# Performance work log

Hardware: AMD Instinct MI355X
Metric: run time of the kernel (lower is better)

The kernel has to match this reference:

```python
import jax, jax.numpy as jnp
import numpy as np

N = 65536      # nodes
E = 262144     # edges per metapath
K = 8          # sampled edges per node
NMP = 2        # metapaths (n_mp)
DEPTH = 2      # layers
H = 4          # heads
D = 256        # prep_len / hidden (= H*PH)
PH = 64        # per-head output dim
ED = 64        # raw edge embedding dim


def setup_inputs() -> dict:
    key = jax.random.key(0)
    ks = jax.random.split(key, 16)
    s = 1.0 / np.sqrt(D)
    return {
        "feats": jax.random.normal(ks[0], (N, D), jnp.float32),
        "edge_emb": jax.random.normal(ks[1], (NMP, E, ED), jnp.float32),
        "edge_node_adj": jax.random.randint(ks[2], (NMP, E, 2), 0, N, dtype=jnp.int32),
        "node2edge_idx": jax.random.randint(ks[3], (NMP, N, K), 0, E, dtype=jnp.int32),
        "W_prep0": jax.random.normal(ks[4], (D, D), jnp.float32) * s,
        "W_prep1": jax.random.normal(ks[5], (D, D), jnp.float32) * s,
        "W_eprep": jax.random.normal(ks[6], (NMP, ED, D), jnp.float32) * (1.0 / np.sqrt(ED)),
        "a_e": jax.random.normal(ks[7], (NMP, DEPTH, H, D), jnp.float32) * s,
        "a_n": jax.random.normal(ks[8], (NMP, DEPTH, H, D), jnp.float32) * s,
        "W_e": jax.random.normal(ks[9], (NMP, DEPTH, H, D, PH), jnp.float32) * s,
        "a_s": jax.random.normal(ks[10], (NMP, DEPTH, H, D), jnp.float32) * s,
        "a_edge": jax.random.normal(ks[11], (NMP, DEPTH, H, D), jnp.float32) * s,
        "W_self": jax.random.normal(ks[12], (NMP, DEPTH, H, D, PH), jnp.float32) * s,
        "W_nb": jax.random.normal(ks[13], (NMP, DEPTH, H, D, PH), jnp.float32) * s,
    }


def _forward(feats, edge_emb, edge_node_adj, node2edge_idx,
             W_prep0, W_prep1, W_eprep, a_e, a_n, W_e, a_s, a_edge, W_self, W_nb):
    dummy = feats @ W_prep0     # prep(layer_idx=0)  [N,D]
    base = feats @ W_prep1      # prep(layer_idx=1)  [N,D]
    outputs = []
    for mp in range(NMP):
        x = base
        edges = edge_emb[mp] @ W_eprep[mp]           # [E,D]
        ena = edge_node_adj[mp]                      # [E,2]
        n2e = node2edge_idx[mp]                      # [N,K]
        skips = []
        for L in range(DEPTH):
            # --- edge aggregator: gather 2 endpoint node feats, attend, project ---
            ep = x[ena]                              # [E,2,D] gather
            s_e = jax.nn.leaky_relu(
                jnp.einsum('eqd,hd->ehq', ep, a_n[mp, L])
                + jnp.einsum('ed,hd->eh', edges, a_e[mp, L])[..., None], 0.2)  # [E,H,2]
            alp = jax.nn.softmax(s_e, axis=-1)
            agg = jnp.einsum('ehq,eqd->ehd', alp, ep)                          # [E,H,D]
            e_out = jax.nn.elu(
                jnp.einsum('ehd,hdp->ehp', edges[:, None, :] + agg, W_e[mp, L])
            ).reshape(E, H * PH)                                               # [E,D]
            # --- node aggregator: gather K sampled edge feats (OLD edges), attend ---
            xin = x if L > 0 else dummy              # layer 0 self-feature uses dummy prep
            eg = edges[n2e]                          # [N,K,D] gather
            s_n = jax.nn.leaky_relu(
                jnp.einsum('nd,hd->nh', xin, a_s[mp, L])[:, :, None]
                + jnp.einsum('nkd,hd->nhk', eg, a_edge[mp, L]), 0.2)           # [N,H,K]
            aln = jax.nn.softmax(s_n, axis=-1)
            nag = jnp.einsum('nhk,nkd->nhd', aln, eg)                          # [N,H,D]
            n_out = jax.nn.elu(
                jnp.einsum('nd,hdp->nhp', xin, W_self[mp, L])
                + jnp.einsum('nhd,hdp->nhp', nag, W_nb[mp, L])
            ).reshape(N, H * PH)                                               # [N,D]
            skips.append(n_out)
            x = n_out
            edges = e_out
        outputs.append(jnp.concatenate(skips, axis=-1))   # [N, DEPTH*D]
    return jnp.stack(outputs, axis=0)                     # [NMP, N, DEPTH*D]


def reference(feats, edge_emb, edge_node_adj, node2edge_idx,
              W_prep0, W_prep1, W_eprep, a_e, a_n, W_e, a_s, a_edge, W_self, W_nb):
    return _forward(feats, edge_emb, edge_node_adj, node2edge_idx,
                    W_prep0, W_prep1, W_eprep, a_e, a_n, W_e, a_s, a_edge, W_self, W_nb)
```

## Files before the change

kernel.cpp:

```cpp
#include <hip/hip_runtime.h>

typedef unsigned short ushort_t;
typedef unsigned int uint_t;

#define N_NODES 65536
#define N_EDGES 262144

typedef __attribute__((ext_vector_type(8))) short bf16x8;
typedef __attribute__((ext_vector_type(4))) float f32x4;

__device__ __forceinline__ ushort_t f2b(float x) {
  uint_t u = __float_as_uint(x);
  u += 0x7fffu + ((u >> 16) & 1u);
  return (ushort_t)(u >> 16);
}
__device__ __forceinline__ void dec8(uint4 v, float* f) {
  f[0] = __uint_as_float(v.x << 16); f[1] = __uint_as_float(v.x & 0xffff0000u);
  f[2] = __uint_as_float(v.y << 16); f[3] = __uint_as_float(v.y & 0xffff0000u);
  f[4] = __uint_as_float(v.z << 16); f[5] = __uint_as_float(v.z & 0xffff0000u);
  f[6] = __uint_as_float(v.w << 16); f[7] = __uint_as_float(v.w & 0xffff0000u);
}
__device__ __forceinline__ void dec4(uint2 v, float* f) {
  f[0] = __uint_as_float(v.x << 16); f[1] = __uint_as_float(v.x & 0xffff0000u);
  f[2] = __uint_as_float(v.y << 16); f[3] = __uint_as_float(v.y & 0xffff0000u);
}
__device__ __forceinline__ uint4 enc8(const float* f) {
  uint4 v;
  v.x = (uint_t)f2b(f[0]) | ((uint_t)f2b(f[1]) << 16);
  v.y = (uint_t)f2b(f[2]) | ((uint_t)f2b(f[3]) << 16);
  v.z = (uint_t)f2b(f[4]) | ((uint_t)f2b(f[5]) << 16);
  v.w = (uint_t)f2b(f[6]) | ((uint_t)f2b(f[7]) << 16);
  return v;
}
__device__ __forceinline__ uint2 enc4(const float* f) {
  uint2 v;
  v.x = (uint_t)f2b(f[0]) | ((uint_t)f2b(f[1]) << 16);
  v.y = (uint_t)f2b(f[2]) | ((uint_t)f2b(f[3]) << 16);
  return v;
}
__device__ __forceinline__ void ld8(const float* p, float* f) {
  float4 v0 = *(const float4*)p;
  float4 v1 = *(const float4*)(p + 4);
  f[0]=v0.x; f[1]=v0.y; f[2]=v0.z; f[3]=v0.w;
  f[4]=v1.x; f[5]=v1.y; f[6]=v1.z; f[7]=v1.w;
}

#define ELUF(v) ((v) > 0.f ? (v) : __expf(v) - 1.f)

__device__ __forceinline__ void async16(void* lds, const void* g) {
  __builtin_amdgcn_global_load_lds(
      (const __attribute__((address_space(1))) void*)g,
      (__attribute__((address_space(3))) void*)lds, 16, 0, 0);
}

__global__ void wt_kernel(const float* __restrict__ src, ushort_t* __restrict__ dst,
                          int K, int N) {
  long m = blockIdx.y;
  long base = m * (long)K * N;
  int tid = blockIdx.x * 256 + threadIdx.x;
  if (tid >= K * N) return;
  int k = tid % K, n = tid / K;
  dst[base + (long)n * K + k] = f2b(src[base + (long)k * N + n]);
}

__global__ __launch_bounds__(256, 2) void gemm_mfma(
    const float* __restrict__ A, const ushort_t* __restrict__ Wt,
    ushort_t* __restrict__ outb, int K) {
  __shared__ __align__(16) char smem[4096 + 16384];
  ushort_t (*sA)[32] = (ushort_t(*)[32])smem;
  ushort_t (*sB)[32] = (ushort_t(*)[32])(smem + 4096);
  int t = threadIdx.x, w = t >> 6, l = t & 63;
  long r0 = (long)blockIdx.x * 64;
  f32x4 zero = {0.f, 0.f, 0.f, 0.f};
  f32x4 acc[4][4];
#pragma unroll
  for (int mt = 0; mt < 4; ++mt)
#pragma unroll
    for (int nt = 0; nt < 4; ++nt) acc[mt][nt] = zero;

  for (int kc = 0; kc < K / 32; ++kc) {
    __syncthreads();
    {
      int r = t >> 2, ks8 = (t & 3) * 8;
      float f[8]; ld8(A + (r0 + r) * (long)K + kc * 32 + ks8, f);
      *(uint4*)&sA[r][ks8] = enc8(f);
    }
#pragma unroll
    for (int j = 0; j < 4; ++j) {
      int u = (w * 4 + j) * 64 + l;
      int n = u >> 2, ks = u & 3;
      async16((char*)sB + (w * 4 + j) * 1024, Wt + (long)n * K + kc * 32 + ks * 8);
    }
    __syncthreads();
    bf16x8 af[4], bf[4];
#pragma unroll
    for (int mt = 0; mt < 4; ++mt)
      af[mt] = *(const bf16x8*)&sA[mt * 16 + (l & 15)][(l >> 4) * 8];
#pragma unroll
    for (int nt = 0; nt < 4; ++nt)
      bf[nt] = *(const bf16x8*)&sB[w * 64 + nt * 16 + (l & 15)][(l >> 4) * 8];
#pragma unroll
    for (int mt = 0; mt < 4; ++mt)
#pragma unroll
      for (int nt = 0; nt < 4; ++nt)
        acc[mt][nt] = __builtin_amdgcn_mfma_f32_16x16x32_bf16(af[mt], bf[nt], acc[mt][nt], 0, 0, 0);
  }
#pragma unroll
  for (int mt = 0; mt < 4; ++mt)
#pragma unroll
    for (int nt = 0; nt < 4; ++nt)
#pragma unroll
      for (int i = 0; i < 4; ++i) {
        long row = r0 + mt * 16 + (l >> 4) * 4 + i;
        int col = w * 64 + nt * 16 + (l & 15);
        outb[row * 256 + col] = f2b(acc[mt][nt][i]);
      }
}

__global__ __launch_bounds__(256, 2) void gemm_eproj(
    const ushort_t* __restrict__ A, const ushort_t* __restrict__ Wt,
    const float* __restrict__ a_vec,
    ushort_t* __restrict__ outb, float* __restrict__ sco) {
  __shared__ __align__(16) char smem[4096 + 16384 + 8192];
  ushort_t (*sA)[32]   = (ushort_t(*)[32])smem;
  ushort_t (*sB)[32]   = (ushort_t(*)[32])(smem + 4096);
  ushort_t (*sAe)[256] = (ushort_t(*)[256])(smem + 20480);
  int t = threadIdx.x, w = t >> 6, l = t & 63;
  long r0 = (long)blockIdx.x * 64;

  {
    int row = t >> 4, seg = (t & 15) * 16;
    float f[16];
    if (row < 4) {
      ld8(a_vec + row * 256 + seg, f);
      ld8(a_vec + row * 256 + seg + 8, f + 8);
    } else {
#pragma unroll
      for (int i = 0; i < 16; ++i) f[i] = 0.f;
    }
    *(uint4*)&sAe[row][seg] = enc8(f);
    *(uint4*)&sAe[row][seg + 8] = enc8(f + 8);
  }

  f32x4 zero = {0.f, 0.f, 0.f, 0.f};
  f32x4 acc[4][4];
  f32x4 accs[4];
#pragma unroll
  for (int mt = 0; mt < 4; ++mt) {
    accs[mt] = zero;
#pragma unroll
    for (int nt = 0; nt < 4; ++nt) acc[mt][nt] = zero;
  }

  for (int kc = 0; kc < 8; ++kc) {
    __syncthreads();
    async16((char*)sA + w * 1024, A + (r0 + (t >> 2)) * 256 + kc * 32 + (t & 3) * 8);
#pragma unroll
    for (int j = 0; j < 4; ++j) {
      int u = (w * 4 + j) * 64 + l;
      int n = u >> 2, ks = u & 3;
      async16((char*)sB + (w * 4 + j) * 1024, Wt + (long)n * 256 + kc * 32 + ks * 8);
    }
    __syncthreads();
    bf16x8 af[4], bf[4];
#pragma unroll
    for (int mt = 0; mt < 4; ++mt)
      af[mt] = *(const bf16x8*)&sA[mt * 16 + (l & 15)][(l >> 4) * 8];
#pragma unroll
    for (int nt = 0; nt < 4; ++nt)
      bf[nt] = *(const bf16x8*)&sB[w * 64 + nt * 16 + (l & 15)][(l >> 4) * 8];
#pragma unroll
    for (int mt = 0; mt < 4; ++mt)
#pragma unroll
      for (int nt = 0; nt < 4; ++nt)
        acc[mt][nt] = __builtin_amdgcn_mfma_f32_16x16x32_bf16(af[mt], bf[nt], acc[mt][nt], 0, 0, 0);
    if (w == 0) {
      bf16x8 bs = *(const bf16x8*)&sAe[l & 15][kc * 32 + (l >> 4) * 8];
#pragma unroll
      for (int mt = 0; mt < 4; ++mt)
        accs[mt] = __builtin_amdgcn_mfma_f32_16x16x32_bf16(af[mt], bs, accs[mt], 0, 0, 0);
    }
  }
#pragma unroll
  for (int mt = 0; mt < 4; ++mt)
#pragma unroll
    for (int nt = 0; nt < 4; ++nt)
#pragma unroll
      for (int i = 0; i < 4; ++i) {
        long row = r0 + mt * 16 + (l >> 4) * 4 + i;
        int col = w * 64 + nt * 16 + (l & 15);
        outb[row * 256 + col] = f2b(acc[mt][nt][i]);
      }
  if (w == 0 && (l & 15) < 4) {
#pragma unroll
    for (int mt = 0; mt < 4; ++mt)
#pragma unroll
      for (int i = 0; i < 4; ++i) {
        long row = r0 + mt * 16 + (l >> 4) * 4 + i;
        sco[row * 4 + (l & 15)] = accs[mt][i];
      }
  }
}

__global__ __launch_bounds__(256, 2) void edge_combine(
    const int* __restrict__ ena,
    const ushort_t* __restrict__ eprojE,
    const ushort_t* __restrict__ xprojE,
    const float* __restrict__ xan,
    const float* __restrict__ sea,
    const ushort_t* __restrict__ Wt,
    const float* __restrict__ a_edge,
    ushort_t* __restrict__ outb,
    float* __restrict__ sed) {
  __shared__ __align__(16) char smem[4096 + 16384 + 8192 + 2048 + 512];
  ushort_t (*sY)[32]   = (ushort_t(*)[32])smem;
  ushort_t (*sB)[32]   = (ushort_t(*)[32])(smem + 4096);
  ushort_t (*sAe)[256] = (ushort_t(*)[256])(smem + 20480);
  float (*sAlp)[4][2]  = (float(*)[4][2])(smem + 28672);
  int* sIdx            = (int*)(smem + 30720);
  int t = threadIdx.x, w = t >> 6, l = t & 63;
  long e0 = (long)blockIdx.x * 64;

  {
    int row = t >> 4, seg = (t & 15) * 16;
    float f[16];
    if (row < 4) {
      ld8(a_edge + row * 256 + seg, f);
      ld8(a_edge + row * 256 + seg + 8, f + 8);
    } else {
#pragma unroll
      for (int i = 0; i < 16; ++i) f[i] = 0.f;
    }
    *(uint4*)&sAe[row][seg] = enc8(f);
    *(uint4*)&sAe[row][seg + 8] = enc8(f + 8);
  }
  if (t < 128) sIdx[t] = ena[e0 * 2 + t];
  __syncthreads();

  {
    int e = t >> 2, h = t & 3;
    int n0 = sIdx[2 * e], n1 = sIdx[2 * e + 1];
    float sE = sea[(e0 + e) * 4 + h];
    float s0 = xan[(long)n0 * 4 + h] + sE; s0 = s0 > 0.f ? s0 : 0.2f * s0;
    float s1 = xan[(long)n1 * 4 + h] + sE; s1 = s1 > 0.f ? s1 : 0.2f * s1;
    float mx = fmaxf(s0, s1);
    float g0 = __expf(s0 - mx), g1 = __expf(s1 - mx);
    float inv = 1.f / (g0 + g1);
    sAlp[e][h][0] = g0 * inv;
    sAlp[e][h][1] = g1 * inv;
  }

  int r = t >> 2, c0 = (t & 3) * 8;
  int n0r = sIdx[2 * r], n1r = sIdx[2 * r + 1];
  const ushort_t* pe = eprojE + (e0 + r) * 256 + c0;
  const ushort_t* p0 = xprojE + (long)n0r * 256 + c0;
  const ushort_t* p1 = xprojE + (long)n1r * 256 + c0;

  f32x4 zero = {0.f, 0.f, 0.f, 0.f};
  f32x4 acc[4][4];
  f32x4 accs[4];
#pragma unroll
  for (int mt = 0; mt < 4; ++mt) {
    accs[mt] = zero;
#pragma unroll
    for (int nt = 0; nt < 4; ++nt) acc[mt][nt] = zero;
  }

  for (int kc = 0; kc < 8; ++kc) {
    __syncthreads();
#pragma unroll
    for (int j = 0; j < 4; ++j) {
      int u = (w * 4 + j) * 64 + l;
      int n = u >> 2, ks = u & 3;
      async16((char*)sB + (w * 4 + j) * 1024, Wt + (long)n * 256 + kc * 32 + ks * 8);
    }
    {
      int h = kc >> 1;
      float a0 = sAlp[r][h][0], a1 = sAlp[r][h][1];
      float ep[8], x0[8], x1[8], y[8];
      dec8(*(const uint4*)(pe + kc * 32), ep);
      dec8(*(const uint4*)(p0 + kc * 32), x0);
      dec8(*(const uint4*)(p1 + kc * 32), x1);
#pragma unroll
      for (int d = 0; d < 8; ++d) {
        float v = ep[d] + a0 * x0[d] + a1 * x1[d];
        y[d] = ELUF(v);
      }
      *(uint4*)&sY[r][c0] = enc8(y);
    }
    __syncthreads();
    bf16x8 af[4], bf[4];
#pragma unroll
    for (int mt = 0; mt < 4; ++mt)
      af[mt] = *(const bf16x8*)&sY[mt * 16 + (l & 15)][(l >> 4) * 8];
#pragma unroll
    for (int nt = 0; nt < 4; ++nt)
      bf[nt] = *(const bf16x8*)&sB[w * 64 + nt * 16 + (l & 15)][(l >> 4) * 8];
#pragma unroll
    for (int mt = 0; mt < 4; ++mt)
#pragma unroll
      for (int nt = 0; nt < 4; ++nt)
        acc[mt][nt] = __builtin_amdgcn_mfma_f32_16x16x32_bf16(af[mt], bf[nt], acc[mt][nt], 0, 0, 0);
    if (w == 0) {
      bf16x8 bs = *(const bf16x8*)&sAe[l & 15][kc * 32 + (l >> 4) * 8];
#pragma unroll
      for (int mt = 0; mt < 4; ++mt)
        accs[mt] = __builtin_amdgcn_mfma_f32_16x16x32_bf16(af[mt], bs, accs[mt], 0, 0, 0);
    }
  }
#pragma unroll
  for (int mt = 0; mt < 4; ++mt)
#pragma unroll
    for (int nt = 0; nt < 4; ++nt)
#pragma unroll
      for (int i = 0; i < 4; ++i) {
        long row = e0 + mt * 16 + (l >> 4) * 4 + i;
        int col = w * 64 + nt * 16 + (l & 15);
        outb[row * 256 + col] = f2b(acc[mt][nt][i]);
      }
  if (w == 0 && (l & 15) < 4) {
#pragma unroll
    for (int mt = 0; mt < 4; ++mt)
#pragma unroll
      for (int i = 0; i < 4; ++i) {
        long row = e0 + mt * 16 + (l >> 4) * 4 + i;
        sed[row * 4 + (l & 15)] = accs[mt][i];
      }
  }
}

__global__ __launch_bounds__(256, 2) void node_out(
    const ushort_t* __restrict__ xb,
    const int* __restrict__ n2e,
    const ushort_t* __restrict__ eproj,
    const float* __restrict__ sed,
    const float* __restrict__ a_s,
    const ushort_t* __restrict__ WtS,
    float* __restrict__ outp,
    ushort_t* __restrict__ xout) {
  __shared__ __align__(16) char smem[33280 + 1024 + 4096 + 4096];
  ushort_t (*sX)[32]   = (ushort_t(*)[32])smem;
  ushort_t (*sBs)[32]  = (ushort_t(*)[32])(smem + 2048);
  ushort_t (*sAs)[256] = (ushort_t(*)[256])(smem + 18432);
  float* sOutF         = (float*)smem;
  int*   sIdx          = (int*)(smem + 33280);
  float* sSe           = (float*)(smem + 34304);
  float* sAln          = (float*)(smem + 38400);
  int t = threadIdx.x, w = t >> 6, l = t & 63;
  long n0 = (long)blockIdx.x * 32;

  {
    int e = n2e[n0 * 8 + t];
    sIdx[t] = e;
    *(float4*)&sSe[t * 4] = *(const float4*)(sed + (long)e * 4);
  }
  if (t < 128) {
    int row = t >> 5, dof = (t & 31) * 8;
    float f[8]; ld8(a_s + row * 256 + dof, f);
    *(uint4*)&sAs[row][dof] = enc8(f);
  }

  f32x4 zero = {0.f, 0.f, 0.f, 0.f};
  f32x4 acc[2][4];
#pragma unroll
  for (int mt = 0; mt < 2; ++mt)
#pragma unroll
    for (int nt = 0; nt < 4; ++nt) acc[mt][nt] = zero;
  float ssp = 0.f;
  int sn = t >> 3, shalf = (t & 1) * 16, sh = (t >> 1) & 3;

  for (int kc = 0; kc < 8; ++kc) {
    __syncthreads();
    if (w == 0) {
#pragma unroll
      for (int j = 0; j < 2; ++j) {
        int u = j * 64 + l;
        int r = u >> 2, ks = u & 3;
        async16((char*)sX + j * 1024, xb + (n0 + r) * 256 + kc * 32 + ks * 8);
      }
    }
#pragma unroll
    for (int j = 0; j < 4; ++j) {
      int u = (w * 4 + j) * 64 + l;
      int n = u >> 2, ks = u & 3;
      async16((char*)sBs + (w * 4 + j) * 1024, WtS + (long)n * 256 + kc * 32 + ks * 8);
    }
    __syncthreads();
    bf16x8 ax[2], bs[4];
#pragma unroll
    for (int mt = 0; mt < 2; ++mt)
      ax[mt] = *(const bf16x8*)&sX[mt * 16 + (l & 15)][(l >> 4) * 8];
#pragma unroll
    for (int nt = 0; nt < 4; ++nt)
      bs[nt] = *(const bf16x8*)&sBs[w * 64 + nt * 16 + (l & 15)][(l >> 4) * 8];
#pragma unroll
    for (int mt = 0; mt < 2; ++mt)
#pragma unroll
      for (int nt = 0; nt < 4; ++nt)
        acc[mt][nt] = __builtin_amdgcn_mfma_f32_16x16x32_bf16(ax[mt], bs[nt], acc[mt][nt], 0, 0, 0);
    {
      float xv[16], av[16];
      dec8(*(const uint4*)&sX[sn][shalf], xv);
      dec8(*(const uint4*)&sX[sn][shalf + 8], xv + 8);
      dec8(*(const uint4*)&sAs[sh][kc * 32 + shalf], av);
      dec8(*(const uint4*)&sAs[sh][kc * 32 + shalf + 8], av + 8);
#pragma unroll
      for (int d = 0; d < 16; ++d) ssp += xv[d] * av[d];
    }
  }
  __syncthreads();
#pragma unroll
  for (int mt = 0; mt < 2; ++mt)
#pragma unroll
    for (int nt = 0; nt < 4; ++nt)
#pragma unroll
      for (int i = 0; i < 4; ++i) {
        int row = mt * 16 + (l >> 4) * 4 + i;
        int col = w * 64 + nt * 16 + (l & 15);
        sOutF[row * 260 + col] = acc[mt][nt][i];
      }
  float ssv = ssp + __shfl_xor(ssp, 1, 64);
  if (!(t & 1)) {
    float sv[8], mx = -1e30f;
#pragma unroll
    for (int k = 0; k < 8; ++k) {
      float s = ssv + sSe[(sn * 8 + k) * 4 + sh];
      s = s > 0.f ? s : 0.2f * s;
      sv[k] = s; mx = fmaxf(mx, s);
    }
    float sum = 0.f;
#pragma unroll
    for (int k = 0; k < 8; ++k) { sv[k] = __expf(sv[k] - mx); sum += sv[k]; }
    float inv = 1.f / sum;
#pragma unroll
    for (int k = 0; k < 8; ++k) sAln[(sn * 4 + sh) * 8 + k] = sv[k] * inv;
  }
  __syncthreads();

  int nT = t >> 3, sT = t & 7, hh = sT >> 1, dof = sT * 32;
  float wts[8];
#pragma unroll
  for (int k = 0; k < 8; ++k) wts[k] = sAln[(nT * 4 + hh) * 8 + k];
  int eidx[8];
#pragma unroll
  for (int k = 0; k < 8; ++k) eidx[k] = sIdx[nT * 8 + k];
  float o[32];
#pragma unroll
  for (int j = 0; j < 8; ++j) {
    float4 sv = *(const float4*)&sOutF[nT * 260 + dof + j * 4];
    o[j * 4 + 0] = sv.x; o[j * 4 + 1] = sv.y; o[j * 4 + 2] = sv.z; o[j * 4 + 3] = sv.w;
  }
#pragma unroll
  for (int k = 0; k < 8; ++k) {
    const ushort_t* pr = eproj + (long)eidx[k] * 256 + dof;
    float v[32];
    dec8(*(const uint4*)(pr),      v);
    dec8(*(const uint4*)(pr + 8),  v + 8);
    dec8(*(const uint4*)(pr + 16), v + 16);
    dec8(*(const uint4*)(pr + 24), v + 24);
    float wk = wts[k];
#pragma unroll
    for (int d = 0; d < 32; ++d) o[d] += wk * v[d];
  }
  long row = n0 + nT;
  float res[32];
#pragma unroll
  for (int d = 0; d < 32; ++d) res[d] = ELUF(o[d]);
  float* po = outp + row * 512 + dof;
#pragma unroll
  for (int j = 0; j < 8; ++j) {
    float4 q;
    q.x = res[j * 4 + 0]; q.y = res[j * 4 + 1]; q.z = res[j * 4 + 2]; q.w = res[j * 4 + 3];
    *(float4*)(po + j * 4) = q;
  }
  if (xout) {
#pragma unroll
    for (int j = 0; j < 4; ++j)
      *(uint4*)(xout + row * 256 + dof + j * 8) = enc8(res + j * 8);
  }
}

extern "C" void kernel_launch(void* const* d_in, const int* in_sizes, int n_in,
                              void* d_out, int out_size, void* d_ws, size_t ws_size,
                              hipStream_t stream) {
  (void)in_sizes; (void)n_in; (void)out_size; (void)ws_size;
  const float* feats  = (const float*)d_in[0];
  const float* eemb   = (const float*)d_in[1];
  const int*   adj    = (const int*)d_in[2];
  const int*   n2e    = (const int*)d_in[3];
  const float* Wp0    = (const float*)d_in[4];
  const float* Wp1    = (const float*)d_in[5];
  const float* Wep    = (const float*)d_in[6];
  const float* a_e    = (const float*)d_in[7];
  const float* a_n    = (const float*)d_in[8];
  const float* W_e    = (const float*)d_in[9];
  const float* a_s    = (const float*)d_in[10];
  const float* a_edge = (const float*)d_in[11];
  const float* W_self = (const float*)d_in[12];
  const float* W_nb   = (const float*)d_in[13];
  float* out = (float*)d_out;

  char* w = (char*)d_ws;
  ushort_t* dummy_bf = (ushort_t*)w; w += (size_t)N_NODES * 256 * 2;
  ushort_t* base_bf  = (ushort_t*)w; w += (size_t)N_NODES * 256 * 2;
  ushort_t* bufEA    = (ushort_t*)w; w += (size_t)N_EDGES * 256 * 2;
  ushort_t* bufEB    = (ushort_t*)w; w += (size_t)N_EDGES * 256 * 2;
  ushort_t* bufEC    = (ushort_t*)w; w += (size_t)N_EDGES * 256 * 2;
  ushort_t* bufX     = (ushort_t*)w; w += (size_t)N_NODES * 256 * 2;
  float*    sea      = (float*)w;    w += (size_t)N_EDGES * 4 * 4;
  float*    sed0     = (float*)w;    w += (size_t)N_EDGES * 4 * 4;
  float*    sed1     = (float*)w;    w += (size_t)N_EDGES * 4 * 4;
  float*    xan      = (float*)w;    w += (size_t)N_NODES * 4 * 4;
  ushort_t* WtP0     = (ushort_t*)w; w += 256 * 256 * 2;
  ushort_t* WtP1     = (ushort_t*)w; w += 256 * 256 * 2;
  ushort_t* WtEp     = (ushort_t*)w; w += 2 * 256 * 64 * 2;
  ushort_t* WtE      = (ushort_t*)w; w += 16 * 16384 * 2;
  ushort_t* WtS      = (ushort_t*)w; w += 16 * 16384 * 2;
  ushort_t* WtN      = (ushort_t*)w; w += 16 * 16384 * 2;

  wt_kernel<<<dim3(256, 1), 256, 0, stream>>>(Wp0, WtP0, 256, 256);
  wt_kernel<<<dim3(256, 1), 256, 0, stream>>>(Wp1, WtP1, 256, 256);
  wt_kernel<<<dim3(64, 2), 256, 0, stream>>>(Wep, WtEp, 64, 256);
  wt_kernel<<<dim3(64, 16), 256, 0, stream>>>(W_e, WtE, 256, 64);
  wt_kernel<<<dim3(64, 16), 256, 0, stream>>>(W_self, WtS, 256, 64);
  wt_kernel<<<dim3(64, 16), 256, 0, stream>>>(W_nb, WtN, 256, 64);

  gemm_mfma<<<N_NODES / 64, 256, 0, stream>>>(feats, WtP0, dummy_bf, 256);
  gemm_mfma<<<N_NODES / 64, 256, 0, stream>>>(feats, WtP1, base_bf, 256);

  for (int mp = 0; mp < 2; ++mp) {
    const int* adj_mp = adj + (size_t)mp * N_EDGES * 2;
    const int* n2e_mp = n2e + (size_t)mp * N_NODES * 8;
    size_t ao0 = (size_t)(mp * 2 + 0) * 1024, ao1 = (size_t)(mp * 2 + 1) * 1024;
    size_t wo0 = (size_t)(mp * 2 + 0) * 65536, wo1 = (size_t)(mp * 2 + 1) * 65536;

    ushort_t* edgesA  = bufEA;
    ushort_t* eprojE  = bufEB;
    ushort_t* eproj0  = bufEC;
    ushort_t* eprojL1 = bufEA;
    ushort_t* xprojE  = bufX;
    ushort_t* xl1     = bufX;

    gemm_mfma<<<N_EDGES / 64, 256, 0, stream>>>(
        eemb + (size_t)mp * N_EDGES * 64, WtEp + (size_t)mp * 16384, edgesA, 64);
    gemm_eproj<<<N_EDGES / 64, 256, 0, stream>>>(edgesA, WtE + wo0, a_e + ao0, eprojE, sea);
    gemm_eproj<<<N_NODES / 64, 256, 0, stream>>>(base_bf, WtE + wo0, a_n + ao0, xprojE, xan);
    gemm_eproj<<<N_EDGES / 64, 256, 0, stream>>>(edgesA, WtN + wo0, a_edge + ao0, eproj0, sed0);
    edge_combine<<<N_EDGES / 64, 256, 0, stream>>>(adj_mp, eprojE, xprojE, xan, sea,
                                                   WtN + wo1, a_edge + ao1, eprojL1, sed1);
    node_out<<<N_NODES / 32, 256, 0, stream>>>(dummy_bf, n2e_mp, eproj0, sed0,
                                               a_s + ao0, WtS + wo0,
                                               out + (size_t)mp * N_NODES * 512, xl1);
    node_out<<<N_NODES / 32, 256, 0, stream>>>(xl1, n2e_mp, eprojL1, sed1,
                                               a_s + ao1, WtS + wo1,
                                               out + (size_t)mp * N_NODES * 512 + 256,
                                               (ushort_t*)nullptr);
  }
}
```

Baseline: 1.584 ms.

## Fuse edge prep, edge projections and combine into one mega kernel; merge prep GEMMs

Merges the edge embedding prep GEMM, the two layer-0 edge projections (W_e and W_nb with their score vectors) and the edge combine step into a single per-64-edge kernel. The prepped edge tile stays in swizzled LDS instead of being written to and re-read from three full [E,256] bf16 buffers. The two feats prep GEMMs are also merged so the A tile is loaded once. This cuts global memory traffic and launches, but LDS per block grows to about 66KB, which may lower occupancy and serialise more work inside each block.

```diff
diff --git a/kernel.cpp b/kernel.cpp
--- a/kernel.cpp
+++ b/kernel.cpp
@@ -63,47 +63,52 @@
   dst[base + (long)n * K + k] = f2b(src[base + (long)k * N + n]);
 }
 
-__global__ __launch_bounds__(256, 2) void gemm_mfma(
-    const float* __restrict__ A, const ushort_t* __restrict__ Wt,
-    ushort_t* __restrict__ outb, int K) {
-  __shared__ __align__(16) char smem[4096 + 16384];
-  ushort_t (*sA)[32] = (ushort_t(*)[32])smem;
-  ushort_t (*sB)[32] = (ushort_t(*)[32])(smem + 4096);
+__global__ __launch_bounds__(256, 2) void gemm_mfma2(
+    const float* __restrict__ A, const ushort_t* __restrict__ Wt0,
+    const ushort_t* __restrict__ Wt1, ushort_t* __restrict__ out0,
+    ushort_t* __restrict__ out1) {
+  __shared__ __align__(16) char smem[4096 + 16384 + 16384];
+  ushort_t (*sA)[32]  = (ushort_t(*)[32])smem;
+  ushort_t (*sB0)[32] = (ushort_t(*)[32])(smem + 4096);
+  ushort_t (*sB1)[32] = (ushort_t(*)[32])(smem + 20480);
   int t = threadIdx.x, w = t >> 6, l = t & 63;
   long r0 = (long)blockIdx.x * 64;
   f32x4 zero = {0.f, 0.f, 0.f, 0.f};
-  f32x4 acc[4][4];
-#pragma unroll
-  for (int mt = 0; mt < 4; ++mt)
-#pragma unroll
-    for (int nt = 0; nt < 4; ++nt) acc[mt][nt] = zero;
-
-  for (int kc = 0; kc < K / 32; ++kc) {
+  f32x4 acc0[4][4], acc1[4][4];
+#pragma unroll
+  for (int mt = 0; mt < 4; ++mt)
+#pragma unroll
+    for (int nt = 0; nt < 4; ++nt) { acc0[mt][nt] = zero; acc1[mt][nt] = zero; }
+
+  for (int kc = 0; kc < 8; ++kc) {
     __syncthreads();
     {
       int r = t >> 2, ks8 = (t & 3) * 8;
-      float f[8]; ld8(A + (r0 + r) * (long)K + kc * 32 + ks8, f);
+      float f[8]; ld8(A + (r0 + r) * 256 + kc * 32 + ks8, f);
       *(uint4*)&sA[r][ks8] = enc8(f);
     }
 #pragma unroll
     for (int j = 0; j < 4; ++j) {
       int u = (w * 4 + j) * 64 + l;
       int n = u >> 2, ks = u & 3;
-      async16((char*)sB + (w * 4 + j) * 1024, Wt + (long)n * K + kc * 32 + ks * 8);
-    }
-    __syncthreads();
-    bf16x8 af[4], bf[4];
+      async16((char*)sB0 + (w * 4 + j) * 1024, Wt0 + (long)n * 256 + kc * 32 + ks * 8);
+      async16((char*)sB1 + (w * 4 + j) * 1024, Wt1 + (long)n * 256 + kc * 32 + ks * 8);
+    }
+    __syncthreads();
+    bf16x8 af[4];
 #pragma unroll
     for (int mt = 0; mt < 4; ++mt)
       af[mt] = *(const bf16x8*)&sA[mt * 16 + (l & 15)][(l >> 4) * 8];
 #pragma unroll
-    for (int nt = 0; nt < 4; ++nt)
-      bf[nt] = *(const bf16x8*)&sB[w * 64 + nt * 16 + (l & 15)][(l >> 4) * 8];
-#pragma unroll
-    for (int mt = 0; mt < 4; ++mt)
-#pragma unroll
-      for (int nt = 0; nt < 4; ++nt)
-        acc[mt][nt] = __builtin_amdgcn_mfma_f32_16x16x32_bf16(af[mt], bf[nt], acc[mt][nt], 0, 0, 0);
+    for (int nt = 0; nt < 4; ++nt) {
+      bf16x8 b0 = *(const bf16x8*)&sB0[w * 64 + nt * 16 + (l & 15)][(l >> 4) * 8];
+      bf16x8 b1 = *(const bf16x8*)&sB1[w * 64 + nt * 16 + (l & 15)][(l >> 4) * 8];
+#pragma unroll
+      for (int mt = 0; mt < 4; ++mt) {
+        acc0[mt][nt] = __builtin_amdgcn_mfma_f32_16x16x32_bf16(af[mt], b0, acc0[mt][nt], 0, 0, 0);
+        acc1[mt][nt] = __builtin_amdgcn_mfma_f32_16x16x32_bf16(af[mt], b1, acc1[mt][nt], 0, 0, 0);
+      }
+    }
   }
 #pragma unroll
   for (int mt = 0; mt < 4; ++mt)
@@ -113,7 +118,8 @@
       for (int i = 0; i < 4; ++i) {
         long row = r0 + mt * 16 + (l >> 4) * 4 + i;
         int col = w * 64 + nt * 16 + (l & 15);
-        outb[row * 256 + col] = f2b(acc[mt][nt][i]);
+        out0[row * 256 + col] = f2b(acc0[mt][nt][i]);
+        out1[row * 256 + col] = f2b(acc1[mt][nt][i]);
       }
 }
 
@@ -202,31 +208,159 @@
   }
 }
 
-__global__ __launch_bounds__(256, 2) void edge_combine(
+__global__ __launch_bounds__(256, 2) void edge_mega(
+    const float* __restrict__ eemb,
+    const ushort_t* __restrict__ WtEp,
+    const ushort_t* __restrict__ WtN0,
+    const ushort_t* __restrict__ WtE0,
+    const ushort_t* __restrict__ WtN1,
+    const float* __restrict__ a_e0,
+    const float* __restrict__ a_ed0,
+    const float* __restrict__ a_ed1,
     const int* __restrict__ ena,
-    const ushort_t* __restrict__ eprojE,
     const ushort_t* __restrict__ xprojE,
     const float* __restrict__ xan,
-    const float* __restrict__ sea,
-    const ushort_t* __restrict__ Wt,
-    const float* __restrict__ a_edge,
-    ushort_t* __restrict__ outb,
-    float* __restrict__ sed) {
-  __shared__ __align__(16) char smem[4096 + 16384 + 8192 + 2048 + 512];
-  ushort_t (*sY)[32]   = (ushort_t(*)[32])smem;
-  ushort_t (*sB)[32]   = (ushort_t(*)[32])(smem + 4096);
-  ushort_t (*sAe)[256] = (ushort_t(*)[256])(smem + 20480);
-  float (*sAlp)[4][2]  = (float(*)[4][2])(smem + 28672);
-  int* sIdx            = (int*)(smem + 30720);
+    ushort_t* __restrict__ eproj0, float* __restrict__ sed0,
+    ushort_t* __restrict__ eprojL1, float* __restrict__ sed1) {
+  __shared__ __align__(16) char smem[32768 + 16384 + 8192 + 4096 + 1024 + 2048 + 512];
+  char* sEc            = smem;
+  ushort_t (*sB)[32]   = (ushort_t(*)[32])(smem + 32768);
+  ushort_t (*sAe)[256] = (ushort_t(*)[256])(smem + 49152);
+  ushort_t (*sT)[32]   = (ushort_t(*)[32])(smem + 57344);
+  float* sSea          = (float*)(smem + 61440);
+  float (*sAlp)[4][2]  = (float(*)[4][2])(smem + 62464);
+  int* sIdx            = (int*)(smem + 64512);
   int t = threadIdx.x, w = t >> 6, l = t & 63;
   long e0 = (long)blockIdx.x * 64;
 
+  if (t < 128) sIdx[t] = ena[e0 * 2 + t];
+  {
+    int row = t >> 4, seg = (t & 15) * 16;
+    float f[16];
+    if (row < 8) {
+      const float* src = (row < 4 ? a_e0 + row * 256 : a_ed0 + (row - 4) * 256) + seg;
+      ld8(src, f); ld8(src + 8, f + 8);
+    } else {
+#pragma unroll
+      for (int i = 0; i < 16; ++i) f[i] = 0.f;
+    }
+    *(uint4*)&sAe[row][seg] = enc8(f);
+    *(uint4*)&sAe[row][seg + 8] = enc8(f + 8);
+  }
+
+  f32x4 zero = {0.f, 0.f, 0.f, 0.f};
+  f32x4 acc[4][4];
+#pragma unroll
+  for (int mt = 0; mt < 4; ++mt)
+#pragma unroll
+    for (int nt = 0; nt < 4; ++nt) acc[mt][nt] = zero;
+
+  for (int kc = 0; kc < 2; ++kc) {
+    __syncthreads();
+    {
+      int r = t >> 2, ks8 = (t & 3) * 8;
+      float f[8]; ld8(eemb + (e0 + r) * 64 + kc * 32 + ks8, f);
+      *(uint4*)&sT[r][ks8] = enc8(f);
+    }
+#pragma unroll
+    for (int j = 0; j < 4; ++j) {
+      int u = (w * 4 + j) * 64 + l;
+      int n = u >> 2, ks = u & 3;
+      async16((char*)sB + (w * 4 + j) * 1024, WtEp + (long)n * 64 + kc * 32 + ks * 8);
+    }
+    __syncthreads();
+    bf16x8 af[4], bf[4];
+#pragma unroll
+    for (int mt = 0; mt < 4; ++mt)
+      af[mt] = *(const bf16x8*)&sT[mt * 16 + (l & 15)][(l >> 4) * 8];
+#pragma unroll
+    for (int nt = 0; nt < 4; ++nt)
+      bf[nt] = *(const bf16x8*)&sB[w * 64 + nt * 16 + (l & 15)][(l >> 4) * 8];
+#pragma unroll
+    for (int mt = 0; mt < 4; ++mt)
+#pragma unroll
+      for (int nt = 0; nt < 4; ++nt)
+        acc[mt][nt] = __builtin_amdgcn_mfma_f32_16x16x32_bf16(af[mt], bf[nt], acc[mt][nt], 0, 0, 0);
+  }
+#pragma unroll
+  for (int mt = 0; mt < 4; ++mt)
+#pragma unroll
+    for (int nt = 0; nt < 4; ++nt)
+#pragma unroll
+      for (int i = 0; i < 4; ++i) {
+        int row = mt * 16 + (l >> 4) * 4 + i;
+        int col = w * 64 + nt * 16 + (l & 15);
+        int cb = (col >> 3) ^ ((row & 7) << 2);
+        *(ushort_t*)(sEc + row * 512 + cb * 16 + (col & 7) * 2) = f2b(acc[mt][nt][i]);
+      }
+
+  f32x4 accs[4];
+#pragma unroll
+  for (int mt = 0; mt < 4; ++mt) {
+    accs[mt] = zero;
+#pragma unroll
+    for (int nt = 0; nt < 4; ++nt) acc[mt][nt] = zero;
+  }
+  for (int kc = 0; kc < 8; ++kc) {
+    __syncthreads();
+#pragma unroll
+    for (int j = 0; j < 4; ++j) {
+      int u = (w * 4 + j) * 64 + l;
+      int n = u >> 2, ks = u & 3;
+      async16((char*)sB + (w * 4 + j) * 1024, WtN0 + (long)n * 256 + kc * 32 + ks * 8);
+    }
+    __syncthreads();
+    bf16x8 af[4], bf[4];
+#pragma unroll
+    for (int mt = 0; mt < 4; ++mt) {
+      int row = mt * 16 + (l & 15);
+      int cb = (kc * 4 + (l >> 4)) ^ ((row & 7) << 2);
+      af[mt] = *(const bf16x8*)(sEc + row * 512 + cb * 16);
+    }
+#pragma unroll
+    for (int nt = 0; nt < 4; ++nt)
+      bf[nt] = *(const bf16x8*)&sB[w * 64 + nt * 16 + (l & 15)][(l >> 4) * 8];
+#pragma unroll
+    for (int mt = 0; mt < 4; ++mt)
+#pragma unroll
+      for (int nt = 0; nt < 4; ++nt)
+        acc[mt][nt] = __builtin_amdgcn_mfma_f32_16x16x32_bf16(af[mt], bf[nt], acc[mt][nt], 0, 0, 0);
+    if (w == 0) {
+      bf16x8 bs = *(const bf16x8*)&sAe[l & 15][kc * 32 + (l >> 4) * 8];
+#pragma unroll
+      for (int mt = 0; mt < 4; ++mt)
+        accs[mt] = __builtin_amdgcn_mfma_f32_16x16x32_bf16(af[mt], bs, accs[mt], 0, 0, 0);
+    }
+  }
+  __syncthreads();
+#pragma unroll
+  for (int mt = 0; mt < 4; ++mt)
+#pragma unroll
+    for (int nt = 0; nt < 4; ++nt)
+#pragma unroll
+      for (int i = 0; i < 4; ++i) {
+        long row = e0 + mt * 16 + (l >> 4) * 4 + i;
+        int col = w * 64 + nt * 16 + (l & 15);
+        eproj0[row * 256 + col] = f2b(acc[mt][nt][i]);
+      }
+  if (w == 0) {
+    int c = l & 15;
+#pragma unroll
+    for (int mt = 0; mt < 4; ++mt)
+#pragma unroll
+      for (int i = 0; i < 4; ++i) {
+        int row = mt * 16 + (l >> 4) * 4 + i;
+        float v = accs[mt][i];
+        if (c < 4) sSea[row * 4 + c] = v;
+        else if (c < 8) sed0[(e0 + row) * 4 + (c - 4)] = v;
+      }
+  }
   {
     int row = t >> 4, seg = (t & 15) * 16;
     float f[16];
     if (row < 4) {
-      ld8(a_edge + row * 256 + seg, f);
-      ld8(a_edge + row * 256 + seg + 8, f + 8);
+      ld8(a_ed1 + row * 256 + seg, f);
+      ld8(a_ed1 + row * 256 + seg + 8, f + 8);
     } else {
 #pragma unroll
       for (int i = 0; i < 16; ++i) f[i] = 0.f;
@@ -234,13 +368,11 @@
     *(uint4*)&sAe[row][seg] = enc8(f);
     *(uint4*)&sAe[row][seg + 8] = enc8(f + 8);
   }
-  if (t < 128) sIdx[t] = ena[e0 * 2 + t];
   __syncthreads();
-
   {
     int e = t >> 2, h = t & 3;
     int n0 = sIdx[2 * e], n1 = sIdx[2 * e + 1];
-    float sE = sea[(e0 + e) * 4 + h];
+    float sE = sSea[e * 4 + h];
     float s0 = xan[(long)n0 * 4 + h] + sE; s0 = s0 > 0.f ? s0 : 0.2f * s0;
     float s1 = xan[(long)n1 * 4 + h] + sE; s1 = s1 > 0.f ? s1 : 0.2f * s1;
     float mx = fmaxf(s0, s1);
@@ -250,49 +382,88 @@
     sAlp[e][h][1] = g1 * inv;
   }
 
-  int r = t >> 2, c0 = (t & 3) * 8;
-  int n0r = sIdx[2 * r], n1r = sIdx[2 * r + 1];
-  const ushort_t* pe = eprojE + (e0 + r) * 256 + c0;
-  const ushort_t* p0 = xprojE + (long)n0r * 256 + c0;
-  const ushort_t* p1 = xprojE + (long)n1r * 256 + c0;
-
-  f32x4 zero = {0.f, 0.f, 0.f, 0.f};
-  f32x4 acc[4][4];
-  f32x4 accs[4];
-#pragma unroll
-  for (int mt = 0; mt < 4; ++mt) {
-    accs[mt] = zero;
+#pragma unroll
+  for (int mt = 0; mt < 4; ++mt)
 #pragma unroll
     for (int nt = 0; nt < 4; ++nt) acc[mt][nt] = zero;
-  }
-
   for (int kc = 0; kc < 8; ++kc) {
     __syncthreads();
 #pragma unroll
     for (int j = 0; j < 4; ++j) {
       int u = (w * 4 + j) * 64 + l;
       int n = u >> 2, ks = u & 3;
-      async16((char*)sB + (w * 4 + j) * 1024, Wt + (long)n * 256 + kc * 32 + ks * 8);
+      async16((char*)sB + (w * 4 + j) * 1024, WtE0 + (long)n * 256 + kc * 32 + ks * 8);
+    }
+    __syncthreads();
+    bf16x8 af[4], bf[4];
+#pragma unroll
+    for (int mt = 0; mt < 4; ++mt) {
+      int row = mt * 16 + (l & 15);
+      int cb = (kc * 4 + (l >> 4)) ^ ((row & 7) << 2);
+      af[mt] = *(const bf16x8*)(sEc + row * 512 + cb * 16);
+    }
+#pragma unroll
+    for (int nt = 0; nt < 4; ++nt)
+      bf[nt] = *(const bf16x8*)&sB[w * 64 + nt * 16 + (l & 15)][(l >> 4) * 8];
+#pragma unroll
+    for (int mt = 0; mt < 4; ++mt)
+#pragma unroll
+      for (int nt = 0; nt < 4; ++nt)
+        acc[mt][nt] = __builtin_amdgcn_mfma_f32_16x16x32_bf16(af[mt], bf[nt], acc[mt][nt], 0, 0, 0);
+  }
+  __syncthreads();
+#pragma unroll
+  for (int mt = 0; mt < 4; ++mt)
+#pragma unroll
+    for (int nt = 0; nt < 4; ++nt)
+#pragma unroll
+      for (int i = 0; i < 4; ++i) {
+        int row = mt * 16 + (l >> 4) * 4 + i;
+        int col = w * 64 + nt * 16 + (l & 15);
+        int cb = (col >> 3) ^ ((row & 7) << 2);
+        *(ushort_t*)(sEc + row * 512 + cb * 16 + (col & 7) * 2) = f2b(acc[mt][nt][i]);
+      }
+
+#pragma unroll
+  for (int mt = 0; mt < 4; ++mt) {
+    accs[mt] = zero;
+#pragma unroll
+    for (int nt = 0; nt < 4; ++nt) acc[mt][nt] = zero;
+  }
+  int r3 = t >> 2, cq = t & 3;
+  int n0r = sIdx[2 * r3], n1r = sIdx[2 * r3 + 1];
+  const ushort_t* p0 = xprojE + (long)n0r * 256 + cq * 8;
+  const ushort_t* p1 = xprojE + (long)n1r * 256 + cq * 8;
+  float a0h[4], a1h[4];
+#pragma unroll
+  for (int h = 0; h < 4; ++h) { a0h[h] = sAlp[r3][h][0]; a1h[h] = sAlp[r3][h][1]; }
+  for (int kc = 0; kc < 8; ++kc) {
+    __syncthreads();
+#pragma unroll
+    for (int j = 0; j < 4; ++j) {
+      int u = (w * 4 + j) * 64 + l;
+      int n = u >> 2, ks = u & 3;
+      async16((char*)sB + (w * 4 + j) * 1024, WtN1 + (long)n * 256 + kc * 32 + ks * 8);
     }
     {
       int h = kc >> 1;
-      float a0 = sAlp[r][h][0], a1 = sAlp[r][h][1];
+      int cb = (kc * 4 + cq) ^ ((r3 & 7) << 2);
       float ep[8], x0[8], x1[8], y[8];
-      dec8(*(const uint4*)(pe + kc * 32), ep);
+      dec8(*(const uint4*)(sEc + r3 * 512 + cb * 16), ep);
       dec8(*(const uint4*)(p0 + kc * 32), x0);
       dec8(*(const uint4*)(p1 + kc * 32), x1);
 #pragma unroll
       for (int d = 0; d < 8; ++d) {
-        float v = ep[d] + a0 * x0[d] + a1 * x1[d];
+        float v = ep[d] + a0h[h] * x0[d] + a1h[h] * x1[d];
         y[d] = ELUF(v);
       }
-      *(uint4*)&sY[r][c0] = enc8(y);
+      *(uint4*)&sT[r3][cq * 8] = enc8(y);
     }
     __syncthreads();
     bf16x8 af[4], bf[4];
 #pragma unroll
     for (int mt = 0; mt < 4; ++mt)
-      af[mt] = *(const bf16x8*)&sY[mt * 16 + (l & 15)][(l >> 4) * 8];
+      af[mt] = *(const bf16x8*)&sT[mt * 16 + (l & 15)][(l >> 4) * 8];
 #pragma unroll
     for (int nt = 0; nt < 4; ++nt)
       bf[nt] = *(const bf16x8*)&sB[w * 64 + nt * 16 + (l & 15)][(l >> 4) * 8];
@@ -316,7 +487,7 @@
       for (int i = 0; i < 4; ++i) {
         long row = e0 + mt * 16 + (l >> 4) * 4 + i;
         int col = w * 64 + nt * 16 + (l & 15);
-        outb[row * 256 + col] = f2b(acc[mt][nt][i]);
+        eprojL1[row * 256 + col] = f2b(acc[mt][nt][i]);
       }
   if (w == 0 && (l & 15) < 4) {
 #pragma unroll
@@ -324,7 +495,7 @@
 #pragma unroll
       for (int i = 0; i < 4; ++i) {
         long row = e0 + mt * 16 + (l >> 4) * 4 + i;
-        sed[row * 4 + (l & 15)] = accs[mt][i];
+        sed1[row * 4 + (l & 15)] = accs[mt][i];
       }
   }
 }
@@ -503,11 +674,9 @@
   char* w = (char*)d_ws;
   ushort_t* dummy_bf = (ushort_t*)w; w += (size_t)N_NODES * 256 * 2;
   ushort_t* base_bf  = (ushort_t*)w; w += (size_t)N_NODES * 256 * 2;
-  ushort_t* bufEA    = (ushort_t*)w; w += (size_t)N_EDGES * 256 * 2;
-  ushort_t* bufEB    = (ushort_t*)w; w += (size_t)N_EDGES * 256 * 2;
-  ushort_t* bufEC    = (ushort_t*)w; w += (size_t)N_EDGES * 256 * 2;
+  ushort_t* eproj0   = (ushort_t*)w; w += (size_t)N_EDGES * 256 * 2;
+  ushort_t* eprojL1  = (ushort_t*)w; w += (size_t)N_EDGES * 256 * 2;
   ushort_t* bufX     = (ushort_t*)w; w += (size_t)N_NODES * 256 * 2;
-  float*    sea      = (float*)w;    w += (size_t)N_EDGES * 4 * 4;
   float*    sed0     = (float*)w;    w += (size_t)N_EDGES * 4 * 4;
   float*    sed1     = (float*)w;    w += (size_t)N_EDGES * 4 * 4;
   float*    xan      = (float*)w;    w += (size_t)N_NODES * 4 * 4;
@@ -525,8 +694,7 @@
   wt_kernel<<<dim3(64, 16), 256, 0, stream>>>(W_self, WtS, 256, 64);
   wt_kernel<<<dim3(64, 16), 256, 0, stream>>>(W_nb, WtN, 256, 64);
 
-  gemm_mfma<<<N_NODES / 64, 256, 0, stream>>>(feats, WtP0, dummy_bf, 256);
-  gemm_mfma<<<N_NODES / 64, 256, 0, stream>>>(feats, WtP1, base_bf, 256);
+  gemm_mfma2<<<N_NODES / 64, 256, 0, stream>>>(feats, WtP0, WtP1, dummy_bf, base_bf);
 
   for (int mp = 0; mp < 2; ++mp) {
     const int* adj_mp = adj + (size_t)mp * N_EDGES * 2;
@@ -534,20 +702,15 @@
     size_t ao0 = (size_t)(mp * 2 + 0) * 1024, ao1 = (size_t)(mp * 2 + 1) * 1024;
     size_t wo0 = (size_t)(mp * 2 + 0) * 65536, wo1 = (size_t)(mp * 2 + 1) * 65536;
 
-    ushort_t* edgesA  = bufEA;
-    ushort_t* eprojE  = bufEB;
-    ushort_t* eproj0  = bufEC;
-    ushort_t* eprojL1 = bufEA;
-    ushort_t* xprojE  = bufX;
-    ushort_t* xl1     = bufX;
-
-    gemm_mfma<<<N_EDGES / 64, 256, 0, stream>>>(
-        eemb + (size_t)mp * N_EDGES * 64, WtEp + (size_t)mp * 16384, edgesA, 64);
-    gemm_eproj<<<N_EDGES / 64, 256, 0, stream>>>(edgesA, WtE + wo0, a_e + ao0, eprojE, sea);
+    ushort_t* xprojE = bufX;
+    ushort_t* xl1    = bufX;
+
     gemm_eproj<<<N_NODES / 64, 256, 0, stream>>>(base_bf, WtE + wo0, a_n + ao0, xprojE, xan);
-    gemm_eproj<<<N_EDGES / 64, 256, 0, stream>>>(edgesA, WtN + wo0, a_edge + ao0, eproj0, sed0);
-    edge_combine<<<N_EDGES / 64, 256, 0, stream>>>(adj_mp, eprojE, xprojE, xan, sea,
-                                                   WtN + wo1, a_edge + ao1, eprojL1, sed1);
+    edge_mega<<<N_EDGES / 64, 256, 0, stream>>>(
+        eemb + (size_t)mp * N_EDGES * 64, WtEp + (size_t)mp * 16384,
+        WtN + wo0, WtE + wo0, WtN + wo1,
+        a_e + ao0, a_edge + ao0, a_edge + ao1,
+        adj_mp, xprojE, xan, eproj0, sed0, eprojL1, sed1);
     node_out<<<N_NODES / 32, 256, 0, stream>>>(dummy_bf, n2e_mp, eproj0, sed0,
                                                a_s + ao0, WtS + wo0,
                                                out + (size_t)mp * N_NODES * 512, xl1);
```

Result: faster. 1.442 ms (-8.9%).
